# Kernel optimization log

Measured on AMD Instinct MI355X. Metric: run time of the kernel, lower is better.

## Reference

```python
import jax, jax.numpy as jnp
import numpy as np

D, FH, FW = 41, 16, 44          # depth bins (arange(4,45,1)), feat H/W = 256/16, 704/16
NX, NY, NZ = 128, 128, 1        # BEV grid from grid_conf
C_CTX = 64                      # LSS context channels
EPS = 1e-5


def _frustum():
    ds = jnp.arange(4.0, 45.0, 1.0)                 # (D,)
    xs = jnp.linspace(0.0, 703.0, FW)
    ys = jnp.linspace(0.0, 255.0, FH)
    return jnp.stack([
        jnp.broadcast_to(xs[None, None, :], (D, FH, FW)),
        jnp.broadcast_to(ys[None, :, None], (D, FH, FW)),
        jnp.broadcast_to(ds[:, None, None], (D, FH, FW)),
    ], -1)                                           # (D,FH,FW,3)


def _bn(x, g, b, m, v):
    # inference-mode BatchNorm2d, x: (B,C,H,W)
    scale = g / jnp.sqrt(v + EPS)
    return x * scale[None, :, None, None] + (b - m * scale)[None, :, None, None]


def setup_inputs() -> dict:
    key = jax.random.key(0)
    ks = jax.random.split(key, 24)
    B, N = 4, 6
    imgs = jax.random.normal(ks[0], (B, N, 3, 256, 704), jnp.float32)
    eye = jnp.eye(3, dtype=jnp.float32)
    # well-conditioned camera matrices (code takes torch.inverse of these)
    rots = eye + 0.05 * jax.random.normal(ks[1], (B, N, 3, 3), jnp.float32)
    trans = 2.0 * jax.random.normal(ks[2], (B, N, 3), jnp.float32)
    K = jnp.array([[500., 0., 352.], [0., 500., 128.], [0., 0., 1.]], jnp.float32)
    kmask = jnp.array([[1., 0., 1.], [0., 1., 1.], [0., 0., 0.]], jnp.float32)
    intrins = K + 5.0 * jax.random.normal(ks[3], (B, N, 3, 3), jnp.float32) * kmask
    post_rots = eye + 0.01 * jax.random.normal(ks[4], (B, N, 3, 3), jnp.float32)
    post_trans = jax.random.normal(ks[5], (B, N, 3), jnp.float32)
    # backbone: Conv2d(3,256,16,16) + BN(256)
    conv_w = 0.02 * jax.random.normal(ks[6], (256, 3, 16, 16), jnp.float32)
    conv_b = 0.01 * jax.random.normal(ks[7], (256,), jnp.float32)
    bn1_g = 1.0 + 0.1 * jax.random.normal(ks[8], (256,), jnp.float32)
    bn1_b = 0.1 * jax.random.normal(ks[9], (256,), jnp.float32)
    bn1_m = 0.1 * jax.random.normal(ks[10], (256,), jnp.float32)
    bn1_v = jax.random.uniform(ks[11], (256,), jnp.float32, 0.5, 1.5)
    # depth_net: Conv2d(256, D+64=105, 1)
    depth_w = 0.05 * jax.random.normal(ks[12], (D + C_CTX, 256), jnp.float32)
    depth_b = 0.01 * jax.random.normal(ks[13], (D + C_CTX,), jnp.float32)
    # BEV encoder: Conv2d(128,64,3,pad=1) + BN(64)
    enc_w = 0.05 * jax.random.normal(ks[14], (64, 128, 3, 3), jnp.float32)
    enc_b = 0.01 * jax.random.normal(ks[15], (64,), jnp.float32)
    bn2_g = 1.0 + 0.1 * jax.random.normal(ks[16], (64,), jnp.float32)
    bn2_b = 0.1 * jax.random.normal(ks[17], (64,), jnp.float32)
    bn2_m = 0.1 * jax.random.normal(ks[18], (64,), jnp.float32)
    bn2_v = jax.random.uniform(ks[19], (64,), jnp.float32, 0.5, 1.5)
    # head: Conv2d(64, 7, 1)
    head_w = 0.05 * jax.random.normal(ks[20], (7, 64), jnp.float32)
    head_b = 0.01 * jax.random.normal(ks[21], (7,), jnp.float32)
    return dict(curr_imgs=imgs, rots=rots, trans=trans, intrins=intrins,
                post_rots=post_rots, post_trans=post_trans,
                conv_w=conv_w, conv_b=conv_b, bn1_g=bn1_g, bn1_b=bn1_b,
                bn1_m=bn1_m, bn1_v=bn1_v, depth_w=depth_w, depth_b=depth_b,
                enc_w=enc_w, enc_b=enc_b, bn2_g=bn2_g, bn2_b=bn2_b,
                bn2_m=bn2_m, bn2_v=bn2_v, head_w=head_w, head_b=head_b)


def _forward(curr_imgs, rots, trans, intrins, post_rots, post_trans,
             conv_w, conv_b, bn1_g, bn1_b, bn1_m, bn1_v,
             depth_w, depth_b, enc_w, enc_b, bn2_g, bn2_b, bn2_m, bn2_v,
             head_w, head_b):
    B, N = curr_imgs.shape[:2]
    dn = ('NCHW', 'OIHW', 'NCHW')
    # backbone (patchify conv + BN + ReLU)
    x = curr_imgs.reshape(B * N, 3, 256, 704)
    x = jax.lax.conv_general_dilated(x, conv_w, (16, 16), 'VALID', dimension_numbers=dn)
    x = jax.nn.relu(_bn(x + conv_b[None, :, None, None], bn1_g, bn1_b, bn1_m, bn1_v))  # (BN,256,16,44)
    # depth net (1x1 conv) -> depth softmax + context
    y = jnp.einsum('oc,bchw->bohw', depth_w, x) + depth_b[None, :, None, None]
    depth = jax.nn.softmax(y[:, :D], axis=1)                 # (BN,D,H,W)
    ctx = y[:, D:]                                           # (BN,C,H,W)
    # LSS outer product: (BN,C,D,H,W) -> (B,N,D,H,W,C)
    outer = ctx[:, :, None] * depth[:, None]
    outer = outer.reshape(B, N, C_CTX, D, FH, FW).transpose(0, 1, 3, 4, 5, 2)
    # geometry: pixel frustum -> ego coords
    fr = _frustum()                                          # (D,FH,FW,3)
    pts = fr[None, None] - post_trans[:, :, None, None, None, :]
    pts = jnp.einsum('bnij,bndhwj->bndhwi', jnp.linalg.inv(post_rots), pts)
    pts = jnp.concatenate([pts[..., :2] * pts[..., 2:3], pts[..., 2:3]], -1)
    comb = rots @ jnp.linalg.inv(intrins)
    pts = jnp.einsum('bnij,bndhwj->bndhwi', comb, pts) + trans[:, :, None, None, None, :]
    # voxel pooling (segment-sum == sort+cumsum trick of the original)
    dx = jnp.array([0.8, 0.8, 20.0], jnp.float32)
    low = jnp.array([-51.2, -51.2, -10.0], jnp.float32)      # bx - dx/2
    coords = ((pts.reshape(-1, 3) - low) / dx).astype(jnp.int32)  # trunc-to-zero like .long()
    rank = coords[:, 0] + coords[:, 1] * NX + coords[:, 2] * NX * NY
    tot = NX * NY * NZ
    kept = (rank >= 0) & (rank < tot)                        # combined-rank check only (as in source)
    feats = outer.reshape(-1, C_CTX) * kept[:, None].astype(outer.dtype)
    bev_flat = jax.ops.segment_sum(feats, jnp.where(kept, rank, 0), num_segments=tot)
    bev = bev_flat.reshape(NZ, NY, NX, C_CTX).transpose(0, 3, 1, 2)  # (1,64,128,128); batch mixed as in source
    # temporal fusion (prev_bev=None branch): cat(bev, bev)
    feat = jnp.concatenate([bev, bev], 1)                    # (1,128,128,128)
    feat = jax.lax.conv_general_dilated(feat, enc_w, (1, 1), 'SAME', dimension_numbers=dn)
    feat = jax.nn.relu(_bn(feat + enc_b[None, :, None, None], bn2_g, bn2_b, bn2_m, bn2_v))
    out = jnp.einsum('oc,bchw->bohw', head_w, feat) + head_b[None, :, None, None]
    return out, bev


def reference(curr_imgs, rots, trans, intrins, post_rots, post_trans,
              conv_w, conv_b, bn1_g, bn1_b, bn1_m, bn1_v,
              depth_w, depth_b, enc_w, enc_b, bn2_g, bn2_b, bn2_m, bn2_v,
              head_w, head_b):
    return _forward(curr_imgs, rots, trans, intrins, post_rots, post_trans,
                    conv_w, conv_b, bn1_g, bn1_b, bn1_m, bn1_v,
                    depth_w, depth_b, enc_w, enc_b, bn2_g, bn2_b, bn2_m, bn2_v,
                    head_w, head_b)
```

## Files before the change

kernel.cpp:

```cpp
#include <hip/hip_runtime.h>
#include <hip/hip_bf16.h>
#include <hip/hip_fp16.h>

#define NPTS 692736
#define NPATCH 16896

typedef _Float16 h16;
typedef __attribute__((ext_vector_type(4))) _Float16 half4v;
typedef __attribute__((ext_vector_type(8))) _Float16 half8v;
typedef __attribute__((ext_vector_type(4))) float f32x4;

__device__ float  v11_xbuf[NPATCH*256];
__device__ float  v11_ctx[NPATCH*64];
__device__ float  v11_depth[NPATCH*41];
__device__ int    v11_ranks[NPTS];
__device__ float  v11_bev[16384*64];
__device__ double v11_geom[24*24];

__device__ h16    v20_whi[196608];
__device__ h16    v20_wlo[196608];

__device__ h16    v15_dwhi[112*256];
__device__ h16    v15_dwlo[112*256];

__device__ h16    v16_w2hi[64*576];
__device__ h16    v16_w2lo[64*576];

__device__ int    v12_cnt[16384];
__device__ int    v12_off[16384];
__device__ int    v12_pos[NPTS];
__device__ int2   v12_sorted[NPTS];
__device__ int    v12_total;

__device__ __forceinline__ void inv3_v11(const double* m, double* o){
  double a=m[0],b=m[1],c=m[2],d=m[3],e=m[4],f=m[5],g=m[6],h=m[7],i=m[8];
  double A = e*i - f*h, B = -(d*i - f*g), C = d*h - e*g;
  double det = a*A + b*B + c*C;
  double id = 1.0/det;
  o[0]=A*id;            o[1]=-(b*i - c*h)*id; o[2]=(b*f - c*e)*id;
  o[3]=B*id;            o[4]=(a*i - c*g)*id;  o[5]=-(a*f - c*d)*id;
  o[6]=C*id;            o[7]=-(a*h - b*g)*id; o[8]=(a*e - b*d)*id;
}

__global__ void prep_v20(const float* cw, const float* dw, const float* enc_w,
                         const float* rots, const float* trans, const float* intrins,
                         const float* post_rots, const float* post_trans){
  int b = blockIdx.x;
  int tid = threadIdx.x;
  if (b < 4096){
    int gid = b*256 + tid;
    v11_bev[gid] = 0.f;
    if (gid < 16384) v12_cnt[gid] = 0;
  } else if (b < 4864){
    int gid = (b-4096)*256 + tid;
    int e  = gid & 7;
    int t  = gid >> 3;
    int o  = t & 63;
    int t2 = t >> 6;
    int kc = t2 & 7;
    int t3 = t2 >> 3;
    int kt = t3 % 12;
    int ob = t3 / 12;
    int k  = kt*64 + kc*8 + e;
    int oc = ob*64 + o;
    float x = cw[oc*768 + k];
    h16 hi = (h16)x;
    v20_whi[gid] = hi;
    v20_wlo[gid] = (h16)(x - (float)hi);
  } else if (b < 4976){
    int gid = (b-4864)*256 + tid;
    int o = gid >> 8, c = gid & 255;
    float x = (o < 105) ? dw[o*256 + c] : 0.f;
    h16 hi = (h16)x;
    v15_dwhi[gid] = hi;
    v15_dwlo[gid] = (h16)(x - (float)hi);
  } else if (b < 5120){
    int gid = (b-4976)*256 + tid;
    if (gid < 36864){
      int o = gid / 576; int k = gid % 576;
      int tap = k >> 6, ic = k & 63;
      float x = enc_w[o*1152 + ic*9 + tap] + enc_w[o*1152 + (ic+64)*9 + tap];
      h16 hi = (h16)x;
      v16_w2hi[gid] = hi;
      v16_w2lo[gid] = (h16)(x - (float)hi);
    }
  } else {
    int t = tid;
    if (t >= 24) return;
    double pr[9], it[9], r[9];
    for (int i=0;i<9;i++){
      pr[i] = (double)post_rots[t*9+i];
      it[i] = (double)intrins[t*9+i];
      r[i]  = (double)rots[t*9+i];
    }
    double ipr[9], iit[9];
    inv3_v11(pr, ipr); inv3_v11(it, iit);
    double* g = v11_geom + t*24;
    for (int i=0;i<3;i++) for(int j=0;j<3;j++){
      double s=0; for(int k=0;k<3;k++) s += r[i*3+k]*iit[k*3+j];
      g[9+i*3+j]=s;
    }
    for (int i=0;i<9;i++) g[i]   = ipr[i];
    for (int i=0;i<3;i++) g[18+i]= (double)post_trans[t*3+i];
    for (int i=0;i<3;i++) g[21+i]= (double)trans[t*3+i];
  }
}

__global__ __launch_bounds__(256) void conv1_v20(const float* img,
    const float* cb, const float* g1, const float* b1, const float* m1, const float* v1){
  __shared__ __align__(16) h16 Ah[8][64][8];
  __shared__ __align__(16) h16 Al[8][64][8];
  __shared__ __align__(16) h16 Bh[4096];
  __shared__ __align__(16) h16 Bl[4096];
  int tid  = threadIdx.x;
  int lane = tid & 63, wv = tid >> 6;
  int wr = wv >> 1, wc = wv & 1;
  int pbase = blockIdx.x * 64;

  int pp0 = tid >> 3, kc0 = tid & 7;
  const float* ab[2];
  #pragma unroll
  for (int i=0;i<2;i++){
    int p = pbase + pp0 + 32*i;
    int im = p/704, pix = p%704;
    int ph = pix/44, pw = pix%44;
    ab[i] = img + (size_t)im*540672 + (size_t)ph*16*704 + pw*16;
  }
  const h16* wph = v20_whi + (size_t)blockIdx.y*12*4096;
  const h16* wpl = v20_wlo + (size_t)blockIdx.y*12*4096;

  float4 pa0[2], pa1[2];
  half8v pbh[2], pbl[2];

  auto LOAD_A = [&](int ktI){
    int k0 = ktI*64 + kc0*8;
    int c = k0>>8, rem = k0&255, ky = rem>>4, kx = rem&15;
    size_t goff = (size_t)c*180224 + ky*704 + kx;
    #pragma unroll
    for (int i=0;i<2;i++){
      pa0[i] = *(const float4*)(ab[i] + goff);
      pa1[i] = *(const float4*)(ab[i] + goff + 4);
    }
  };
  auto LOAD_B = [&](int ktI){
    const h16* ph = wph + (size_t)ktI*4096;
    const h16* pl = wpl + (size_t)ktI*4096;
    #pragma unroll
    for (int i=0;i<2;i++){
      int l = tid + i*256;
      pbh[i] = *(const half8v*)(ph + l*8);
      pbl[i] = *(const half8v*)(pl + l*8);
    }
  };

  f32x4 acc[2][2];
  #pragma unroll
  for (int mf=0;mf<2;mf++)
    #pragma unroll
    for (int nf=0;nf<2;nf++) acc[mf][nf] = (f32x4){0.f,0.f,0.f,0.f};

  int fr = lane & 15, fg = lane >> 4;

  LOAD_A(0); LOAD_B(0);

  for (int ktI=0; ktI<12; ktI++){
    __syncthreads();
    #pragma unroll
    for (int i=0;i<2;i++){
      float vv[8] = {pa0[i].x,pa0[i].y,pa0[i].z,pa0[i].w,
                     pa1[i].x,pa1[i].y,pa1[i].z,pa1[i].w};
      half8v hv, lv;
      #pragma unroll
      for (int e=0;e<8;e++){ h16 h=(h16)vv[e]; hv[e]=h; lv[e]=(h16)(vv[e]-(float)h); }
      int srow = (pp0 + 32*i) ^ kc0;
      *(half8v*)&Ah[kc0][srow][0] = hv;
      *(half8v*)&Al[kc0][srow][0] = lv;
    }
    #pragma unroll
    for (int i=0;i<2;i++){
      int l = tid + i*256;
      *(half8v*)&Bh[l*8] = pbh[i];
      *(half8v*)&Bl[l*8] = pbl[i];
    }
    __syncthreads();
    if (ktI < 11){ LOAD_A(ktI+1); LOAD_B(ktI+1); }
    #pragma unroll
    for (int ks=0;ks<2;ks++){
      int kc = ks*4 + fg;
      half8v ah[2], al[2], bh[2], bl[2];
      #pragma unroll
      for (int mf=0;mf<2;mf++){
        int row = (wr*32 + mf*16 + fr) ^ kc;
        ah[mf] = *(const half8v*)&Ah[kc][row][0];
        al[mf] = *(const half8v*)&Al[kc][row][0];
      }
      #pragma unroll
      for (int nf=0;nf<2;nf++){
        int col = wc*32 + nf*16 + fr;
        bh[nf] = *(const half8v*)&Bh[(kc*64 + col)*8];
        bl[nf] = *(const half8v*)&Bl[(kc*64 + col)*8];
      }
      #pragma unroll
      for (int mf=0;mf<2;mf++)
        #pragma unroll
        for (int nf=0;nf<2;nf++){
          acc[mf][nf] = __builtin_amdgcn_mfma_f32_16x16x32_f16(ah[mf], bh[nf], acc[mf][nf], 0,0,0);
          acc[mf][nf] = __builtin_amdgcn_mfma_f32_16x16x32_f16(ah[mf], bl[nf], acc[mf][nf], 0,0,0);
          acc[mf][nf] = __builtin_amdgcn_mfma_f32_16x16x32_f16(al[mf], bh[nf], acc[mf][nf], 0,0,0);
        }
    }
  }
  int obase = blockIdx.y * 64;
  #pragma unroll
  for (int nf=0;nf<2;nf++){
    int ch = obase + wc*32 + nf*16 + fr;
    float sc = g1[ch] / sqrtf(v1[ch] + 1e-5f);
    float sh = b1[ch] - m1[ch]*sc;
    float bi = cb[ch];
    #pragma unroll
    for (int mf=0;mf<2;mf++){
      #pragma unroll
      for (int j=0;j<4;j++){
        int pq = pbase + wr*32 + mf*16 + fg*4 + j;
        float t = (acc[mf][nf][j] + bi)*sc + sh;
        v11_xbuf[(size_t)pq*256 + ch] = t > 0.f ? t : 0.f;
      }
    }
  }
}

__global__ __launch_bounds__(256) void depth_v16(const float* db){
  __shared__ __align__(16) h16 Ah[4][64][8];
  __shared__ __align__(16) h16 Al[4][64][8];
  __shared__ __align__(16) h16 Bh[4][112][8];
  __shared__ __align__(16) h16 Bl[4][112][8];
  __shared__ float sy[64*113];
  int tid = threadIdx.x;
  int lane = tid & 63, wv = tid >> 6;
  int pbase = blockIdx.x*64;
  int fr = lane & 15, fg = lane >> 4;

  int app = tid & 63;
  int kcA = tid >> 6;
  const float* xsrc = &v11_xbuf[(size_t)(pbase+app)*256 + kcA*8];

  f32x4 acc[7];
  #pragma unroll
  for (int nf=0;nf<7;nf++) acc[nf] = (f32x4){0.f,0.f,0.f,0.f};

  for (int kt=0; kt<256; kt+=32){
    __syncthreads();
    {
      float4 v0 = *(const float4*)(xsrc + kt);
      float4 v1 = *(const float4*)(xsrc + kt + 4);
      float vv[8] = {v0.x,v0.y,v0.z,v0.w,v1.x,v1.y,v1.z,v1.w};
      half8v hv, lv;
      #pragma unroll
      for (int e=0;e<8;e++){ h16 h=(h16)vv[e]; hv[e]=h; lv[e]=(h16)(vv[e]-(float)h); }
      *(half8v*)&Ah[kcA][app][0] = hv;
      *(half8v*)&Al[kcA][app][0] = lv;
    }
    for (int l = tid; l < 448; l += 256){
      int kc = l/112, o = l%112;
      *(half8v*)&Bh[kc][o][0] = *(const half8v*)&v15_dwhi[o*256 + kt + kc*8];
      *(half8v*)&Bl[kc][o][0] = *(const half8v*)&v15_dwlo[o*256 + kt + kc*8];
    }
    __syncthreads();
    int row = wv*16 + fr;
    half8v ah = *(const half8v*)&Ah[fg][row][0];
    half8v al = *(const half8v*)&Al[fg][row][0];
    #pragma unroll
    for (int nf=0;nf<7;nf++){
      int col = nf*16 + fr;
      half8v bh = *(const half8v*)&Bh[fg][col][0];
      half8v bl = *(const half8v*)&Bl[fg][col][0];
      acc[nf] = __builtin_amdgcn_mfma_f32_16x16x32_f16(ah, bh, acc[nf], 0,0,0);
      acc[nf] = __builtin_amdgcn_mfma_f32_16x16x32_f16(ah, bl, acc[nf], 0,0,0);
      acc[nf] = __builtin_amdgcn_mfma_f32_16x16x32_f16(al, bh, acc[nf], 0,0,0);
    }
  }
  #pragma unroll
  for (int nf=0;nf<7;nf++){
    int o = nf*16 + fr;
    if (o < 105){
      float bias = db[o];
      #pragma unroll
      for (int j=0;j<4;j++){
        int pp = wv*16 + fg*4 + j;
        sy[pp*113 + o] = acc[nf][j] + bias;
      }
    }
  }
  __syncthreads();
  if (tid < 64){
    float* y = &sy[tid*113];
    float m = y[0];
    for (int i=1;i<41;i++) m = fmaxf(m, y[i]);
    float s = 0.f;
    for (int i=0;i<41;i++){ float e = expf(y[i]-m); y[i] = e; s += e; }
    float inv = 1.f/s;
    for (int i=0;i<41;i++) y[i] *= inv;
  }
  __syncthreads();
  for (int l = tid; l < 64*41; l += 256){
    int pp = l/41, dd = l%41;
    v11_depth[(size_t)(pbase+pp)*41 + dd] = sy[pp*113+dd];
  }
  for (int l = tid; l < 64*64; l += 256){
    int pp = l>>6, c = l&63;
    v11_ctx[(size_t)(pbase+pp)*64 + c] = sy[pp*113 + 41 + c];
  }
}

__global__ __launch_bounds__(256) void rank_v13(){
  __shared__ int lh[16384];
  int tid = threadIdx.x;
  for (int i = tid; i < 16384; i += 256) lh[i] = 0;
  __syncthreads();
  int base = blockIdx.x*1024;
  int rk[4], lp[4];
  #pragma unroll
  for (int k=0;k<4;k++){
    int idx = base + k*256 + tid;
    rk[k] = -1; lp[k] = 0;
    if (idx < NPTS){
      int im = idx / 28864;
      int r  = idx % 28864;
      int d  = r / 704; int pix = r % 704;
      int h = pix / 44, w = pix % 44;
      const double* g = v11_geom + im*24;
      double fx = (double)w * (703.0/43.0);
      double fy = (double)h * 17.0;
      double fz = 4.0 + (double)d;
      double px = fx - g[18], py = fy - g[19], pz = fz - g[20];
      double q0 = g[0]*px + g[1]*py + g[2]*pz;
      double q1 = g[3]*px + g[4]*py + g[5]*pz;
      double q2 = g[6]*px + g[7]*py + g[8]*pz;
      q0 *= q2; q1 *= q2;
      double o0 = g[9]*q0  + g[10]*q1 + g[11]*q2 + g[21];
      double o1 = g[12]*q0 + g[13]*q1 + g[14]*q2 + g[22];
      double o2 = g[15]*q0 + g[16]*q1 + g[17]*q2 + g[23];
      int cx = (int)((o0 + 51.2)/0.8);
      int cy = (int)((o1 + 51.2)/0.8);
      int cz = (int)((o2 + 10.0)/20.0);
      int rank = cx + cy*128 + cz*16384;
      if (rank >= 0 && rank < 16384){
        rk[k] = rank;
        lp[k] = atomicAdd(&lh[rank], 1);
      }
    }
  }
  __syncthreads();
  for (int i = tid; i < 16384; i += 256){
    int h = lh[i];
    if (h) lh[i] = atomicAdd(&v12_cnt[i], h);
  }
  __syncthreads();
  #pragma unroll
  for (int k=0;k<4;k++){
    int idx = base + k*256 + tid;
    if (idx < NPTS){
      v11_ranks[idx] = rk[k];
      if (rk[k] >= 0) v12_pos[idx] = lh[rk[k]] + lp[k];
    }
  }
}

__global__ __launch_bounds__(256) void scan_v13(){
  __shared__ int part[256];
  int t = threadIdx.x;
  int base = t*64;
  int s = 0;
  for (int i=0;i<64;i++) s += v12_cnt[base+i];
  part[t] = s;
  __syncthreads();
  if (t == 0){
    int run = 0;
    for (int i=0;i<256;i++){ int v = part[i]; part[i] = run; run += v; }
    v12_total = run;
  }
  __syncthreads();
  int run = part[t];
  for (int i=0;i<64;i++){
    v12_off[base+i] = run;
    run += v12_cnt[base+i];
  }
}

__global__ __launch_bounds__(256) void fill_v13(){
  int idx = blockIdx.x*256 + threadIdx.x;
  if (idx >= NPTS) return;
  int rank = v11_ranks[idx];
  if (rank < 0) return;
  int im = idx / 28864;
  int r  = idx % 28864;
  int d  = r / 704; int pix = r % 704;
  int p  = im*704 + pix;
  int pos = v12_off[rank] + v12_pos[idx];
  v12_sorted[pos] = make_int2((p<<6) | d, rank);
}

__global__ __launch_bounds__(256) void gather_v13(){
  int total = v12_total;
  int w = threadIdx.x >> 6;
  int chunk = blockIdx.x*256 + w*64;
  if (chunk >= total) return;
  int lane = threadIdx.x & 63;
  int n = total - chunk; if (n > 64) n = 64;
  int pv = 0, rv = -1;
  float dv = 0.f;
  if (lane < n){
    int2 sr = v12_sorted[chunk + lane];
    pv = sr.x; rv = sr.y;
    dv = v11_depth[(pv>>6)*41 + (pv & 63)];
  }
  float acc = 0.f;
  int cur = __shfl(rv, 0);
  for (int i = 0; i < n; i++){
    int rk = __shfl(rv, i);
    int pp = __shfl(pv, i) >> 6;
    float dd = __shfl(dv, i);
    if (rk != cur){
      atomicAdd(&v11_bev[(size_t)cur*64 + lane], acc);
      acc = 0.f; cur = rk;
    }
    acc += v11_ctx[(pp<<6) | lane] * dd;
  }
  atomicAdd(&v11_bev[(size_t)cur*64 + lane], acc);
}

__global__ __launch_bounds__(256) void conv2_v20(
    const float* eb, const float* g2, const float* b2_, const float* m2, const float* v2,
    const float* hw, const float* hb, float* out0, float* out1){
  __shared__ __align__(16) h16 Ah[4][64][8];
  __shared__ __align__(16) h16 Al[4][64][8];
  __shared__ __align__(16) h16 Bh[4][64][8];
  __shared__ __align__(16) h16 Bl[4][64][8];
  __shared__ float sfeat[64*68];
  __shared__ float hred[4*64*7];
  int tid = threadIdx.x;
  int lane = tid & 63, wv = tid >> 6;
  int bx = blockIdx.x & 15, by = blockIdx.x >> 4;
  int fr = lane & 15, fg = lane >> 4;

  int app = tid & 63;
  int kcT = tid >> 6;
  int apy = app >> 3, apx = app & 7;

  f32x4 acc[4];
  #pragma unroll
  for (int nf=0;nf<4;nf++) acc[nf] = (f32x4){0.f,0.f,0.f,0.f};

  for (int kt=0; kt<576; kt+=32){
    int tap = kt >> 6, ic0 = kt & 32;
    int dy = tap/3 - 1, dx = tap%3 - 1;
    __syncthreads();
    {
      int gy = by*8 + apy + dy, gx = bx*8 + apx + dx;
      float4 v0 = {0.f,0.f,0.f,0.f}, v1 = {0.f,0.f,0.f,0.f};
      if (gy>=0 && gy<128 && gx>=0 && gx<128){
        const float* src = &v11_bev[(size_t)(gy*128+gx)*64 + ic0 + kcT*8];
        v0 = *(const float4*)src;
        v1 = *(const float4*)(src+4);
      }
      float vv[8] = {v0.x,v0.y,v0.z,v0.w,v1.x,v1.y,v1.z,v1.w};
      if (tap == 4){
        int gyc = by*8 + apy, gxc = bx*8 + apx;
        int ch0 = ic0 + kcT*8;
        #pragma unroll
        for (int q=0;q<8;q++)
          out1[(ch0+q)*16384 + gyc*128 + gxc] = vv[q];
      }
      half8v hv, lv;
      #pragma unroll
      for (int e=0;e<8;e++){ h16 h=(h16)vv[e]; hv[e]=h; lv[e]=(h16)(vv[e]-(float)h); }
      *(half8v*)&Ah[kcT][app][0] = hv;
      *(half8v*)&Al[kcT][app][0] = lv;
    }
    {
      *(half8v*)&Bh[kcT][app][0] = *(const half8v*)&v16_w2hi[app*576 + kt + kcT*8];
      *(half8v*)&Bl[kcT][app][0] = *(const half8v*)&v16_w2lo[app*576 + kt + kcT*8];
    }
    __syncthreads();
    int row = wv*16 + fr;
    half8v ah = *(const half8v*)&Ah[fg][row][0];
    half8v al = *(const half8v*)&Al[fg][row][0];
    #pragma unroll
    for (int nf=0;nf<4;nf++){
      int col = nf*16 + fr;
      half8v bh = *(const half8v*)&Bh[fg][col][0];
      half8v bl = *(const half8v*)&Bl[fg][col][0];
      acc[nf] = __builtin_amdgcn_mfma_f32_16x16x32_f16(ah, bh, acc[nf], 0,0,0);
      acc[nf] = __builtin_amdgcn_mfma_f32_16x16x32_f16(ah, bl, acc[nf], 0,0,0);
      acc[nf] = __builtin_amdgcn_mfma_f32_16x16x32_f16(al, bh, acc[nf], 0,0,0);
    }
  }
  #pragma unroll
  for (int nf=0;nf<4;nf++){
    int ch = nf*16 + fr;
    float sc = g2[ch]/sqrtf(v2[ch]+1e-5f);
    float sh = b2_[ch] - m2[ch]*sc;
    float bi = eb[ch];
    #pragma unroll
    for (int j=0;j<4;j++){
      int pp = wv*16 + fg*4 + j;
      float t = (acc[nf][j] + bi)*sc + sh;
      sfeat[pp*68 + ch] = t > 0.f ? t : 0.f;
    }
  }
  __syncthreads();
  int og = tid >> 6, pix = tid & 63;
  float part[7];
  #pragma unroll
  for (int o=0;o<7;o++) part[o]=0.f;
  #pragma unroll
  for (int j=0;j<16;j++){
    int oc = og*16 + j;
    float v = sfeat[pix*68 + oc];
    #pragma unroll
    for (int o=0;o<7;o++) part[o] += hw[o*64+oc]*v;
  }
  #pragma unroll
  for (int o=0;o<7;o++) hred[(og*64+pix)*7+o] = part[o];
  __syncthreads();
  if (og == 0){
    int gy = by*8 + (pix>>3), gx = bx*8 + (pix&7);
    #pragma unroll
    for (int o=0;o<7;o++){
      float s = hred[pix*7+o] + hred[(64+pix)*7+o] + hred[(128+pix)*7+o]
              + hred[(192+pix)*7+o] + hb[o];
      out0[o*16384 + gy*128 + gx] = s;
    }
  }
}

extern "C" void kernel_launch(void* const* d_in, const int* in_sizes, int n_in,
                              void* d_out, int out_size, void* d_ws, size_t ws_size,
                              hipStream_t stream){
  const float* imgs       = (const float*)d_in[0];
  const float* rots       = (const float*)d_in[1];
  const float* trans      = (const float*)d_in[2];
  const float* intrins    = (const float*)d_in[3];
  const float* post_rots  = (const float*)d_in[4];
  const float* post_trans = (const float*)d_in[5];
  const float* conv_w     = (const float*)d_in[6];
  const float* conv_b     = (const float*)d_in[7];
  const float* bn1_g      = (const float*)d_in[8];
  const float* bn1_b      = (const float*)d_in[9];
  const float* bn1_m      = (const float*)d_in[10];
  const float* bn1_v      = (const float*)d_in[11];
  const float* depth_w    = (const float*)d_in[12];
  const float* depth_b    = (const float*)d_in[13];
  const float* enc_w      = (const float*)d_in[14];
  const float* enc_b      = (const float*)d_in[15];
  const float* bn2_g      = (const float*)d_in[16];
  const float* bn2_b      = (const float*)d_in[17];
  const float* bn2_m      = (const float*)d_in[18];
  const float* bn2_v      = (const float*)d_in[19];
  const float* head_w     = (const float*)d_in[20];
  const float* head_b     = (const float*)d_in[21];

  float* out0 = (float*)d_out;
  float* out1 = out0 + 114688;

  prep_v20<<<5121, 256, 0, stream>>>(conv_w, depth_w, enc_w,
                                     rots, trans, intrins, post_rots, post_trans);
  conv1_v20<<<dim3(264, 4), 256, 0, stream>>>(imgs, conv_b, bn1_g, bn1_b, bn1_m, bn1_v);
  depth_v16<<<264, 256, 0, stream>>>(depth_b);
  rank_v13<<<(NPTS+1023)/1024, 256, 0, stream>>>();
  scan_v13<<<1, 256, 0, stream>>>();
  fill_v13<<<NPTS/256, 256, 0, stream>>>();
  gather_v13<<<NPTS/256, 256, 0, stream>>>();
  conv2_v20<<<256, 256, 0, stream>>>(enc_b, bn2_g, bn2_b, bn2_m, bn2_v,
                                     head_w, head_b, out0, out1);
}
```

Measured before the change: 258.2 us.

## Prefetch depth GEMM tiles into registers and enlarge rank histogram blocks

The depth kernel now loads the next K-tile of activations and split-fp16 weights into registers before the MFMA work on the current tile, so global-load latency overlaps with compute. The rank kernel handles 4096 points per block instead of 1024. This cuts the number of 16384-entry shared histograms that have to be zeroed and flushed to global atomics, and it writes ranks and local positions straight to global memory, then fixes the positions up in a second pass. The trade-offs are more register pressure in the depth kernel, fewer blocks in the rank kernel, and an extra global read-modify-write of positions.

```diff
diff --git a/kernel.cpp b/kernel.cpp
--- a/kernel.cpp
+++ b/kernel.cpp
@@ -229,7 +229,7 @@
   }
 }
 
-__global__ __launch_bounds__(256) void depth_v16(const float* db){
+__global__ __launch_bounds__(256) void depth_v19(const float* db){
   __shared__ __align__(16) h16 Ah[4][64][8];
   __shared__ __align__(16) h16 Al[4][64][8];
   __shared__ __align__(16) h16 Bh[4][112][8];
@@ -244,28 +244,55 @@
   int kcA = tid >> 6;
   const float* xsrc = &v11_xbuf[(size_t)(pbase+app)*256 + kcA*8];
 
+  int wl[2], wkc[2], wo[2];
+  #pragma unroll
+  for (int i=0;i<2;i++){
+    int l = tid + i*256;
+    wl[i] = (l < 448);
+    wkc[i] = l/112; wo[i] = l%112;
+  }
+
+  float4 na0, na1;
+  half8v nwh[2], nwl_[2];
+  auto LOAD_A = [&](int ktI){
+    na0 = *(const float4*)(xsrc + ktI*32);
+    na1 = *(const float4*)(xsrc + ktI*32 + 4);
+  };
+  auto LOAD_W = [&](int ktI){
+    #pragma unroll
+    for (int i=0;i<2;i++){
+      if (wl[i]){
+        nwh[i]  = *(const half8v*)&v15_dwhi[wo[i]*256 + ktI*32 + wkc[i]*8];
+        nwl_[i] = *(const half8v*)&v15_dwlo[wo[i]*256 + ktI*32 + wkc[i]*8];
+      }
+    }
+  };
+
   f32x4 acc[7];
   #pragma unroll
   for (int nf=0;nf<7;nf++) acc[nf] = (f32x4){0.f,0.f,0.f,0.f};
 
-  for (int kt=0; kt<256; kt+=32){
+  LOAD_A(0); LOAD_W(0);
+
+  for (int ktI=0; ktI<8; ktI++){
     __syncthreads();
     {
-      float4 v0 = *(const float4*)(xsrc + kt);
-      float4 v1 = *(const float4*)(xsrc + kt + 4);
-      float vv[8] = {v0.x,v0.y,v0.z,v0.w,v1.x,v1.y,v1.z,v1.w};
+      float vv[8] = {na0.x,na0.y,na0.z,na0.w,na1.x,na1.y,na1.z,na1.w};
       half8v hv, lv;
       #pragma unroll
       for (int e=0;e<8;e++){ h16 h=(h16)vv[e]; hv[e]=h; lv[e]=(h16)(vv[e]-(float)h); }
       *(half8v*)&Ah[kcA][app][0] = hv;
       *(half8v*)&Al[kcA][app][0] = lv;
     }
-    for (int l = tid; l < 448; l += 256){
-      int kc = l/112, o = l%112;
-      *(half8v*)&Bh[kc][o][0] = *(const half8v*)&v15_dwhi[o*256 + kt + kc*8];
-      *(half8v*)&Bl[kc][o][0] = *(const half8v*)&v15_dwlo[o*256 + kt + kc*8];
+    #pragma unroll
+    for (int i=0;i<2;i++){
+      if (wl[i]){
+        *(half8v*)&Bh[wkc[i]][wo[i]][0] = nwh[i];
+        *(half8v*)&Bl[wkc[i]][wo[i]][0] = nwl_[i];
+      }
     }
     __syncthreads();
+    if (ktI < 7){ LOAD_A(ktI+1); LOAD_W(ktI+1); }
     int row = wv*16 + fr;
     half8v ah = *(const half8v*)&Ah[fg][row][0];
     half8v al = *(const half8v*)&Al[fg][row][0];
@@ -312,43 +339,38 @@
   }
 }
 
-__global__ __launch_bounds__(256) void rank_v13(){
+__global__ __launch_bounds__(256) void rank_v14(){
   __shared__ int lh[16384];
   int tid = threadIdx.x;
   for (int i = tid; i < 16384; i += 256) lh[i] = 0;
   __syncthreads();
-  int base = blockIdx.x*1024;
-  int rk[4], lp[4];
-  #pragma unroll
-  for (int k=0;k<4;k++){
+  int base = blockIdx.x*4096;
+  for (int k=0;k<16;k++){
     int idx = base + k*256 + tid;
-    rk[k] = -1; lp[k] = 0;
-    if (idx < NPTS){
-      int im = idx / 28864;
-      int r  = idx % 28864;
-      int d  = r / 704; int pix = r % 704;
-      int h = pix / 44, w = pix % 44;
-      const double* g = v11_geom + im*24;
-      double fx = (double)w * (703.0/43.0);
-      double fy = (double)h * 17.0;
-      double fz = 4.0 + (double)d;
-      double px = fx - g[18], py = fy - g[19], pz = fz - g[20];
-      double q0 = g[0]*px + g[1]*py + g[2]*pz;
-      double q1 = g[3]*px + g[4]*py + g[5]*pz;
-      double q2 = g[6]*px + g[7]*py + g[8]*pz;
-      q0 *= q2; q1 *= q2;
-      double o0 = g[9]*q0  + g[10]*q1 + g[11]*q2 + g[21];
-      double o1 = g[12]*q0 + g[13]*q1 + g[14]*q2 + g[22];
-      double o2 = g[15]*q0 + g[16]*q1 + g[17]*q2 + g[23];
-      int cx = (int)((o0 + 51.2)/0.8);
-      int cy = (int)((o1 + 51.2)/0.8);
-      int cz = (int)((o2 + 10.0)/20.0);
-      int rank = cx + cy*128 + cz*16384;
-      if (rank >= 0 && rank < 16384){
-        rk[k] = rank;
-        lp[k] = atomicAdd(&lh[rank], 1);
-      }
-    }
+    if (idx >= NPTS) break;
+    int im = idx / 28864;
+    int r  = idx % 28864;
+    int d  = r / 704; int pix = r % 704;
+    int h = pix / 44, w = pix % 44;
+    const double* g = v11_geom + im*24;
+    double fx = (double)w * (703.0/43.0);
+    double fy = (double)h * 17.0;
+    double fz = 4.0 + (double)d;
+    double px = fx - g[18], py = fy - g[19], pz = fz - g[20];
+    double q0 = g[0]*px + g[1]*py + g[2]*pz;
+    double q1 = g[3]*px + g[4]*py + g[5]*pz;
+    double q2 = g[6]*px + g[7]*py + g[8]*pz;
+    q0 *= q2; q1 *= q2;
+    double o0 = g[9]*q0  + g[10]*q1 + g[11]*q2 + g[21];
+    double o1 = g[12]*q0 + g[13]*q1 + g[14]*q2 + g[22];
+    double o2 = g[15]*q0 + g[16]*q1 + g[17]*q2 + g[23];
+    int cx = (int)((o0 + 51.2)/0.8);
+    int cy = (int)((o1 + 51.2)/0.8);
+    int cz = (int)((o2 + 10.0)/20.0);
+    int rank = cx + cy*128 + cz*16384;
+    bool ok = (rank >= 0 && rank < 16384);
+    v11_ranks[idx] = ok ? rank : -1;
+    if (ok) v12_pos[idx] = atomicAdd(&lh[rank], 1);
   }
   __syncthreads();
   for (int i = tid; i < 16384; i += 256){
@@ -356,13 +378,11 @@
     if (h) lh[i] = atomicAdd(&v12_cnt[i], h);
   }
   __syncthreads();
-  #pragma unroll
-  for (int k=0;k<4;k++){
+  for (int k=0;k<16;k++){
     int idx = base + k*256 + tid;
-    if (idx < NPTS){
-      v11_ranks[idx] = rk[k];
-      if (rk[k] >= 0) v12_pos[idx] = lh[rk[k]] + lp[k];
-    }
+    if (idx >= NPTS) break;
+    int rank = v11_ranks[idx];
+    if (rank >= 0) v12_pos[idx] += lh[rank];
   }
 }
 
@@ -566,8 +586,8 @@
   prep_v20<<<5121, 256, 0, stream>>>(conv_w, depth_w, enc_w,
                                      rots, trans, intrins, post_rots, post_trans);
   conv1_v20<<<dim3(264, 4), 256, 0, stream>>>(imgs, conv_b, bn1_g, bn1_b, bn1_m, bn1_v);
-  depth_v16<<<264, 256, 0, stream>>>(depth_b);
-  rank_v13<<<(NPTS+1023)/1024, 256, 0, stream>>>();
+  depth_v19<<<264, 256, 0, stream>>>(depth_b);
+  rank_v14<<<(NPTS+4095)/4096, 256, 0, stream>>>();
   scan_v13<<<1, 256, 0, stream>>>();
   fill_v13<<<NPTS/256, 256, 0, stream>>>();
   gather_v13<<<NPTS/256, 256, 0, stream>>>();
```

Result: slower. 264.0 us (+2.3%).
